# Optimization experiments

Measured on AMD Instinct MI355X. Metric: run time of the kernel, lower is better.

## Reference

```python
import jax, jax.numpy as jnp
import numpy as np

N_HEADS = 16
ROPE_BASE = 10000.0


def apply_rope(x):
    # x: [B, H, T, D]; rotate interleaved pairs along last dim, positions along T
    B, H, T, D = x.shape
    half = D // 2
    inv_freq = 1.0 / (ROPE_BASE ** (jnp.arange(0, half, dtype=jnp.float32) * 2.0 / D))
    angles = jnp.arange(T, dtype=jnp.float32)[:, None] * inv_freq[None, :]  # [T, half]
    cos = jnp.cos(angles).astype(x.dtype)  # [T, half]
    sin = jnp.sin(angles).astype(x.dtype)
    xp = x.reshape(B, H, T, half, 2)
    x1, x2 = xp[..., 0], xp[..., 1]
    out = jnp.stack([x1 * cos - x2 * sin, x1 * sin + x2 * cos], axis=-1)
    return out.reshape(B, H, T, D)


def setup_inputs() -> dict:
    key = jax.random.key(0)
    k1, k2, k3 = jax.random.split(key, 3)
    C = 1024
    x = jax.random.normal(k1, (2, 2048, C), dtype=jnp.float32)
    w_qkv = jax.random.normal(k2, (C, 3 * C), dtype=jnp.float32) * (1.0 / np.sqrt(C))
    w_out = jax.random.normal(k3, (C, C), dtype=jnp.float32) * (1.0 / np.sqrt(C))
    return {"x": x, "w_qkv": w_qkv, "w_out": w_out}


def reference(x, w_qkv, w_out):
    B, T, C = x.shape
    H = N_HEADS
    D = C // H
    qkv = (x @ w_qkv).reshape(B, T, 3, H, D)
    q, k, v = qkv[:, :, 0], qkv[:, :, 1], qkv[:, :, 2]  # [B, T, H, D]
    q = jnp.transpose(q, (0, 2, 1, 3))  # [B, H, T, D]
    k = jnp.transpose(k, (0, 2, 1, 3))
    v = jnp.transpose(v, (0, 2, 1, 3))
    q = apply_rope(q)
    k = apply_rope(k)
    scale = 1.0 / np.sqrt(D)
    scores = jnp.einsum('bhqd,bhkd->bhqk', q, k) * scale
    causal = jnp.tril(jnp.ones((T, T), dtype=bool))
    scores = jnp.where(causal, scores, jnp.finfo(scores.dtype).min)
    attn = jax.nn.softmax(scores, axis=-1)
    out = jnp.einsum('bhqk,bhkd->bhqd', attn, v)  # [B, H, T, D]
    out = jnp.transpose(out, (0, 2, 1, 3)).reshape(B, T, C)
    return out @ w_out
```

## Files before the change

kernel.cpp:

```cpp
#include <hip/hip_runtime.h>
#include <hip/hip_bf16.h>

typedef __attribute__((ext_vector_type(8))) short v8s;
typedef __attribute__((ext_vector_type(4))) float v4f;
typedef __attribute__((ext_vector_type(16))) float v16f;

typedef const __attribute__((address_space(1))) void* gas_ptr;
typedef __attribute__((address_space(3))) void* las_ptr;

#define MFMA16(a, b, c) __builtin_amdgcn_mfma_f32_16x16x32_bf16((a), (b), (c), 0, 0, 0)
#define MFMA32(a, b, c) __builtin_amdgcn_mfma_f32_32x32x16_bf16((a), (b), (c), 0, 0, 0)

__device__ __forceinline__ void gload_lds16(const void* g, void* l) {
  __builtin_amdgcn_global_load_lds((gas_ptr)g, (las_ptr)l, 16, 0, 0);
}

__device__ __forceinline__ unsigned short f2bf(float f) {
  unsigned int u = __float_as_uint(f);
  u += 0x7FFFu + ((u >> 16) & 1u);
  return (unsigned short)(u >> 16);
}
__device__ __forceinline__ float bf2f(unsigned short h) {
  return __uint_as_float(((unsigned int)h) << 16);
}

__device__ __forceinline__ unsigned cvt_pk_bf16(float lo, float hi) {
  unsigned r;
  asm("v_cvt_pk_bf16_f32 %0, %1, %2" : "=v"(r) : "v"(lo), "v"(hi));
  return r;
}

__global__ __launch_bounds__(256) void k_convert(const float* __restrict__ in,
                                                 unsigned short* __restrict__ out,
                                                 float2* __restrict__ tab, int n4) {
  if ((int)blockIdx.x >= 4096) {
    int base = ((int)blockIdx.x - 4096) * 256 + threadIdx.x;
#pragma unroll
    for (int e = 0; e < 8; ++e) {
      int n = base * 8 + e;
      int pos = n >> 5, i = n & 31;
      float invf = exp2f(-(float)i * 0.41524101186092034f);
      float ang = (float)pos * invf;
      float s, cc;
      sincosf(ang, &s, &cc);
      tab[n] = make_float2(cc, s);
    }
    return;
  }
  int i = blockIdx.x * 256 + threadIdx.x;
  if (i >= n4) return;
  float4 v = ((const float4*)in)[i];
  ushort4 o;
  o.x = f2bf(v.x); o.y = f2bf(v.y); o.z = f2bf(v.z); o.w = f2bf(v.w);
  ((ushort4*)out)[i] = o;
}

__global__ __launch_bounds__(256) void k_transpose_convert(const float* __restrict__ in,
                                                           unsigned short* __restrict__ out,
                                                           int R, int C) {
  __shared__ __attribute__((aligned(16))) unsigned short tb[64 * 72];
  const int r0 = blockIdx.y * 64, c0 = blockIdx.x * 64;
  const int tid = threadIdx.x;
#pragma unroll
  for (int j = 0; j < 4; ++j) {
    int slot = tid + 256 * j;
    int row = slot >> 4, q4 = (slot & 15) * 4;
    float4 v = *(const float4*)&in[(size_t)(r0 + row) * C + c0 + q4];
    ushort4 o;
    o.x = f2bf(v.x); o.y = f2bf(v.y); o.z = f2bf(v.z); o.w = f2bf(v.w);
    *(ushort4*)&tb[row * 72 + q4] = o;
  }
  __syncthreads();
#pragma unroll
  for (int j = 0; j < 4; ++j) {
    int slot = tid + 256 * j;
    int crow = slot >> 4, t4 = (slot & 15) * 4;
    ushort4 o;
    o.x = tb[(t4 + 0) * 72 + crow];
    o.y = tb[(t4 + 1) * 72 + crow];
    o.z = tb[(t4 + 2) * 72 + crow];
    o.w = tb[(t4 + 3) * 72 + crow];
    *(ushort4*)&out[(size_t)(c0 + crow) * R + r0 + t4] = o;
  }
}

template <bool F32OUT, int BN, int WAVES_M, int WAVES_N>
__global__ __launch_bounds__(256) void k_gemm(const unsigned short* __restrict__ A,
                                              const unsigned short* __restrict__ Bt,
                                              void* __restrict__ Cout,
                                              int M, int N, int K) {
  constexpr int WM = 128 / (WAVES_M * 16);
  constexpr int WN = BN / (WAVES_N * 16);
  __shared__ __attribute__((aligned(16))) unsigned short As[128 * 32];
  __shared__ __attribute__((aligned(16))) unsigned short Bs[BN * 32];
  const int tid = threadIdx.x;
  const int w = tid >> 6, l = tid & 63, g = l >> 4, c = l & 15;
  const int wr = w / WAVES_N, wc = w % WAVES_N;

  const int nwg = gridDim.x * gridDim.y;
  const int orig = blockIdx.y * gridDim.x + blockIdx.x;
  const int wgid = (orig & 7) * (nwg >> 3) + (orig >> 3);
  const int mt = (wgid / gridDim.x) * 128;
  const int nt = (wgid % gridDim.x) * BN;

  const int rowc = l >> 2, kslot = (l & 3) * 8;

  v4f acc[WM][WN];
#pragma unroll
  for (int m = 0; m < WM; ++m)
#pragma unroll
    for (int n = 0; n < WN; ++n) acc[m][n] = (v4f){0.f, 0.f, 0.f, 0.f};

  constexpr int NCHUNK = 8 + BN / 16;
  for (int kt = 0; kt < K; kt += 32) {
    __syncthreads();
#pragma unroll
    for (int ch = 0; ch < NCHUNK; ch += 4) {
      int cc = ch + w;
      if (cc < 8)
        gload_lds16(&A[(size_t)(mt + cc * 16 + rowc) * K + kt + kslot], &As[cc * 512]);
      else
        gload_lds16(&Bt[(size_t)(nt + (cc - 8) * 16 + rowc) * K + kt + kslot],
                    &Bs[(cc - 8) * 512]);
    }
    __syncthreads();
    v8s af[WM], bfr[WN];
#pragma unroll
    for (int m = 0; m < WM; ++m)
      af[m] = *(const v8s*)&As[(wr * (WM * 16) + m * 16 + c) * 32 + g * 8];
#pragma unroll
    for (int n = 0; n < WN; ++n)
      bfr[n] = *(const v8s*)&Bs[(wc * (WN * 16) + n * 16 + c) * 32 + g * 8];
#pragma unroll
    for (int m = 0; m < WM; ++m)
#pragma unroll
      for (int n = 0; n < WN; ++n)
        acc[m][n] = MFMA16(af[m], bfr[n], acc[m][n]);
  }

#pragma unroll
  for (int m = 0; m < WM; ++m)
#pragma unroll
    for (int n = 0; n < WN; ++n)
#pragma unroll
      for (int r = 0; r < 4; ++r) {
        int row = mt + wr * (WM * 16) + m * 16 + g * 4 + r;
        int col = nt + wc * (WN * 16) + n * 16 + c;
        if (F32OUT)
          ((float*)Cout)[(size_t)row * N + col] = acc[m][n][r];
        else
          ((unsigned short*)Cout)[(size_t)row * N + col] = f2bf(acc[m][n][r]);
      }
}

__global__ __launch_bounds__(256) void k_gemm_qkv(const unsigned short* __restrict__ A,
                                                  const unsigned short* __restrict__ Bt,
                                                  const float2* __restrict__ tab,
                                                  unsigned short* __restrict__ qp,
                                                  unsigned short* __restrict__ kp,
                                                  unsigned short* __restrict__ vp) {
  __shared__ __attribute__((aligned(16))) unsigned short As[128 * 32];
  __shared__ __attribute__((aligned(16))) unsigned short Bs[128 * 32];
  __shared__ __attribute__((aligned(16))) unsigned short T[128 * 136];
  const int tid = threadIdx.x;
  const int w = tid >> 6, l = tid & 63, g = l >> 4, c = l & 15;
  const int wr = w >> 1, wc = w & 1;

  const int nwg = 768;
  const int orig = blockIdx.y * 24 + blockIdx.x;
  const int wgid = (orig & 7) * (nwg >> 3) + (orig >> 3);
  const int mt = (wgid / 24) * 128;
  const int nt = (wgid % 24) * 128;

  const int rowc = l >> 2, kslot = (l & 3) * 8;

  v4f acc[4][4];
#pragma unroll
  for (int m = 0; m < 4; ++m)
#pragma unroll
    for (int n = 0; n < 4; ++n) acc[m][n] = (v4f){0.f, 0.f, 0.f, 0.f};

  for (int kt = 0; kt < 1024; kt += 32) {
    __syncthreads();
#pragma unroll
    for (int ch = 0; ch < 16; ch += 4) {
      int cc = ch + w;
      if (cc < 8)
        gload_lds16(&A[(size_t)(mt + cc * 16 + rowc) * 1024 + kt + kslot], &As[cc * 512]);
      else
        gload_lds16(&Bt[(size_t)(nt + (cc - 8) * 16 + rowc) * 1024 + kt + kslot],
                    &Bs[(cc - 8) * 512]);
    }
    __syncthreads();
    v8s af[4], bfr[4];
#pragma unroll
    for (int m = 0; m < 4; ++m)
      af[m] = *(const v8s*)&As[(wr * 64 + m * 16 + c) * 32 + g * 8];
#pragma unroll
    for (int n = 0; n < 4; ++n)
      bfr[n] = *(const v8s*)&Bs[(wc * 64 + n * 16 + c) * 32 + g * 8];
#pragma unroll
    for (int m = 0; m < 4; ++m)
#pragma unroll
      for (int n = 0; n < 4; ++n)
        acc[m][n] = MFMA16(af[m], bfr[n], acc[m][n]);
  }

#pragma unroll
  for (int m = 0; m < 4; ++m)
#pragma unroll
    for (int n = 0; n < 4; ++n)
#pragma unroll
      for (int r = 0; r < 4; ++r)
        T[(wr * 64 + m * 16 + g * 4 + r) * 136 + wc * 64 + n * 16 + c] = f2bf(acc[m][n][r]);
  __syncthreads();

  const int which = nt >> 10;
  const int h0 = (nt & 1023) >> 6;
  const int b = mt >> 11;
  const int posbase = mt & 2047;

  if (which < 2) {
    const float qsc = which ? 1.0f : 0.18033688011112042f;
    unsigned short* dst = which ? kp : qp;
#pragma unroll
    for (int it = 0; it < 8; ++it) {
      int task = it * 256 + tid;
      int c32t = task & 31;
      int grp = task >> 5;
      int hg = grp & 1, kd = (grp >> 1) & 3, tR = (grp >> 3) & 3, hd2 = grp >> 5;
      int row = tR * 32 + c32t;
      int d0 = kd * 16 + hg * 8;
      int pos = posbase + row;
      v8s vq = *(const v8s*)&T[row * 136 + hd2 * 64 + d0];
      union { unsigned short s[8]; v8s v; } uo;
#pragma unroll
      for (int p = 0; p < 4; ++p) {
        float2 sc = tab[pos * 32 + (d0 >> 1) + p];
        float x1 = bf2f((unsigned short)vq[2 * p]);
        float x2 = bf2f((unsigned short)vq[2 * p + 1]);
        uo.s[2 * p]     = f2bf((x1 * sc.x - x2 * sc.y) * qsc);
        uo.s[2 * p + 1] = f2bf((x1 * sc.y + x2 * sc.x) * qsc);
      }
      int bh = b * 16 + h0 + hd2;
      int tileG = pos >> 5;
      *(v8s*)&dst[(size_t)bh * 131072 + (tileG * 4 + kd) * 512 + (hg * 32 + c32t) * 8] = uo.v;
    }
  } else {
#pragma unroll
    for (int it = 0; it < 8; ++it) {
      int task = it * 256 + tid;
      int lp = task & 63;
      int grp = task >> 6;
      int md = grp & 1, kc = (grp >> 1) & 1, tR = (grp >> 2) & 3, hd2 = grp >> 4;
      int hh2 = lp >> 5, c32d = lp & 31;
      int d = md * 32 + c32d;
      int brow = tR * 32 + kc * 16 + hh2 * 4;
      union { unsigned short s[8]; v8s v; } uo;
#pragma unroll
      for (int jh = 0; jh < 2; ++jh)
#pragma unroll
        for (int e = 0; e < 4; ++e)
          uo.s[jh * 4 + e] = T[(brow + jh * 8 + e) * 136 + hd2 * 64 + d];
      int bh = b * 16 + h0 + hd2;
      int tileG = (posbase >> 5) + tR;
      *(v8s*)&vp[(size_t)bh * 131072 + ((tileG * 2 + kc) * 2 + md) * 512 + lp * 8] = uo.v;
    }
  }
}

__global__ __launch_bounds__(64) void k_attn(const unsigned short* __restrict__ qp,
                                             const unsigned short* __restrict__ kp,
                                             const unsigned short* __restrict__ vp,
                                             unsigned short* __restrict__ ao,
                                             char* __restrict__ part) {
  const int bid = (int)blockIdx.x;
  const int xcd = bid & 7, s2 = bid >> 3;
  const int bh = xcd + 8 * (s2 / 160);
  const int idx = 159 - (s2 % 160);
  int j, s;
  if (idx >= 96)      { j = 48 + ((idx - 96) >> 2); s = (idx - 96) & 3; }
  else if (idx >= 48) { j = 32 + (idx - 48) / 3;    s = (idx - 48) % 3; }
  else if (idx >= 16) { j = 16 + ((idx - 16) >> 1); s = (idx - 16) & 1; }
  else                { j = idx;                    s = 0; }
  const int t0 = s * 16;
  const int t1 = (t0 + 16 < j + 1) ? (t0 + 16) : (j + 1);

  const int l = threadIdx.x;
  const int c32 = l & 31, hh = l >> 5;
  const unsigned short* Qb = qp + (size_t)bh * 131072 + j * 4 * 512;
  const unsigned short* Kb = kp + (size_t)bh * 131072;
  const unsigned short* Vb = vp + (size_t)bh * 131072;

  v8s bq[4];
#pragma unroll
  for (int kd = 0; kd < 4; ++kd) bq[kd] = *(const v8s*)&Qb[kd * 512 + l * 8];

  v16f ot0 = {0,0,0,0,0,0,0,0,0,0,0,0,0,0,0,0};
  v16f ot1 = {0,0,0,0,0,0,0,0,0,0,0,0,0,0,0,0};
  float m2 = -1e30f, lsl = 0.f;

  v8s ak[2][4], av[2][2][2];
#pragma unroll
  for (int kd = 0; kd < 4; ++kd) ak[0][kd] = *(const v8s*)&Kb[((size_t)t0 * 4 + kd) * 512 + l * 8];
#pragma unroll
  for (int kc = 0; kc < 2; ++kc)
#pragma unroll
    for (int md = 0; md < 2; ++md)
      av[0][kc][md] = *(const v8s*)&Vb[(((size_t)t0 * 2 + kc) * 2 + md) * 512 + l * 8];
  if (t0 + 1 < t1) {
#pragma unroll
    for (int kd = 0; kd < 4; ++kd)
      ak[1][kd] = *(const v8s*)&Kb[((size_t)(t0 + 1) * 4 + kd) * 512 + l * 8];
#pragma unroll
    for (int kc = 0; kc < 2; ++kc)
#pragma unroll
      for (int md = 0; md < 2; ++md)
        av[1][kc][md] = *(const v8s*)&Vb[(((size_t)(t0 + 1) * 2 + kc) * 2 + md) * 512 + l * 8];
  }

  int t = t0;
  for (; t + 1 < t1; t += 2) {
    v16f st0 = {0,0,0,0,0,0,0,0,0,0,0,0,0,0,0,0};
    v16f st1 = {0,0,0,0,0,0,0,0,0,0,0,0,0,0,0,0};
    __builtin_amdgcn_s_setprio(1);
#pragma unroll
    for (int kd = 0; kd < 4; ++kd) {
      st0 = MFMA32(ak[0][kd], bq[kd], st0);
      st1 = MFMA32(ak[1][kd], bq[kd], st1);
    }
    __builtin_amdgcn_s_setprio(0);

    if (t + 2 < t1) {
#pragma unroll
      for (int kd = 0; kd < 4; ++kd)
        ak[0][kd] = *(const v8s*)&Kb[((size_t)(t + 2) * 4 + kd) * 512 + l * 8];
    }
    if (t + 3 < t1) {
#pragma unroll
      for (int kd = 0; kd < 4; ++kd)
        ak[1][kd] = *(const v8s*)&Kb[((size_t)(t + 3) * 4 + kd) * 512 + l * 8];
    }

    if (t + 1 == j) {
#pragma unroll
      for (int r = 0; r < 16; ++r) {
        int rloc = (r & 3) + 8 * (r >> 2) + 4 * hh;
        st1[r] = (rloc <= c32) ? st1[r] : -1e30f;
      }
    }

    float a0 = fmaxf(fmaxf(st0[0], st0[1]), fmaxf(st0[2], st0[3]));
    float a1 = fmaxf(fmaxf(st0[4], st0[5]), fmaxf(st0[6], st0[7]));
    float a2 = fmaxf(fmaxf(st0[8], st0[9]), fmaxf(st0[10], st0[11]));
    float a3 = fmaxf(fmaxf(st0[12], st0[13]), fmaxf(st0[14], st0[15]));
    float b0 = fmaxf(fmaxf(st1[0], st1[1]), fmaxf(st1[2], st1[3]));
    float b1 = fmaxf(fmaxf(st1[4], st1[5]), fmaxf(st1[6], st1[7]));
    float b2 = fmaxf(fmaxf(st1[8], st1[9]), fmaxf(st1[10], st1[11]));
    float b3 = fmaxf(fmaxf(st1[12], st1[13]), fmaxf(st1[14], st1[15]));
    float pm = fmaxf(fmaxf(fmaxf(a0, a1), fmaxf(a2, a3)),
                     fmaxf(fmaxf(b0, b1), fmaxf(b2, b3)));
    if (!__all(pm <= m2 + 8.f)) {
      float pmw = fmaxf(pm, __shfl_xor(pm, 32));
      float mn = fmaxf(m2, pmw);
      float al = exp2f(m2 - mn);
      m2 = mn;
      lsl *= al;
      ot0 *= al;
      ot1 *= al;
    }

#pragma unroll
    for (int r = 0; r < 16; ++r) st0[r] = exp2f(st0[r] - m2);
#pragma unroll
    for (int r = 0; r < 16; ++r) st1[r] = exp2f(st1[r] - m2);
    {
      float e0 = (st0[0] + st0[1]) + (st0[2] + st0[3]);
      float e1 = (st0[4] + st0[5]) + (st0[6] + st0[7]);
      float e2 = (st0[8] + st0[9]) + (st0[10] + st0[11]);
      float e3 = (st0[12] + st0[13]) + (st0[14] + st0[15]);
      float f0 = (st1[0] + st1[1]) + (st1[2] + st1[3]);
      float f1 = (st1[4] + st1[5]) + (st1[6] + st1[7]);
      float f2 = (st1[8] + st1[9]) + (st1[10] + st1[11]);
      float f3 = (st1[12] + st1[13]) + (st1[14] + st1[15]);
      lsl += ((e0 + e1) + (e2 + e3)) + ((f0 + f1) + (f2 + f3));
    }

    unsigned wd0[8], wd1[8];
#pragma unroll
    for (int i = 0; i < 8; ++i) wd0[i] = cvt_pk_bf16(st0[2 * i], st0[2 * i + 1]);
#pragma unroll
    for (int i = 0; i < 8; ++i) wd1[i] = cvt_pk_bf16(st1[2 * i], st1[2 * i + 1]);
    union { unsigned u[4]; v8s v; } p00, p01, p10, p11;
    p00.u[0] = wd0[0]; p00.u[1] = wd0[1]; p00.u[2] = wd0[2]; p00.u[3] = wd0[3];
    p01.u[0] = wd0[4]; p01.u[1] = wd0[5]; p01.u[2] = wd0[6]; p01.u[3] = wd0[7];
    p10.u[0] = wd1[0]; p10.u[1] = wd1[1]; p10.u[2] = wd1[2]; p10.u[3] = wd1[3];
    p11.u[0] = wd1[4]; p11.u[1] = wd1[5]; p11.u[2] = wd1[6]; p11.u[3] = wd1[7];

    __builtin_amdgcn_s_setprio(1);
    ot0 = MFMA32(av[0][0][0], p00.v, ot0);
    ot1 = MFMA32(av[0][0][1], p00.v, ot1);
    ot0 = MFMA32(av[0][1][0], p01.v, ot0);
    ot1 = MFMA32(av[0][1][1], p01.v, ot1);
    ot0 = MFMA32(av[1][0][0], p10.v, ot0);
    ot1 = MFMA32(av[1][0][1], p10.v, ot1);
    ot0 = MFMA32(av[1][1][0], p11.v, ot0);
    ot1 = MFMA32(av[1][1][1], p11.v, ot1);
    __builtin_amdgcn_s_setprio(0);

    if (t + 2 < t1) {
#pragma unroll
      for (int kc = 0; kc < 2; ++kc)
#pragma unroll
        for (int md = 0; md < 2; ++md)
          av[0][kc][md] = *(const v8s*)&Vb[(((size_t)(t + 2) * 2 + kc) * 2 + md) * 512 + l * 8];
    }
    if (t + 3 < t1) {
#pragma unroll
      for (int kc = 0; kc < 2; ++kc)
#pragma unroll
        for (int md = 0; md < 2; ++md)
          av[1][kc][md] = *(const v8s*)&Vb[(((size_t)(t + 3) * 2 + kc) * 2 + md) * 512 + l * 8];
    }
  }

  if (t < t1) {
    v16f st = {0,0,0,0,0,0,0,0,0,0,0,0,0,0,0,0};
    __builtin_amdgcn_s_setprio(1);
#pragma unroll
    for (int kd = 0; kd < 4; ++kd) st = MFMA32(ak[0][kd], bq[kd], st);
    __builtin_amdgcn_s_setprio(0);

    if (t == j) {
#pragma unroll
      for (int r = 0; r < 16; ++r) {
        int rloc = (r & 3) + 8 * (r >> 2) + 4 * hh;
        st[r] = (rloc <= c32) ? st[r] : -1e30f;
      }
    }

    float a0 = fmaxf(fmaxf(st[0], st[1]), fmaxf(st[2], st[3]));
    float a1 = fmaxf(fmaxf(st[4], st[5]), fmaxf(st[6], st[7]));
    float a2 = fmaxf(fmaxf(st[8], st[9]), fmaxf(st[10], st[11]));
    float a3 = fmaxf(fmaxf(st[12], st[13]), fmaxf(st[14], st[15]));
    float pm = fmaxf(fmaxf(a0, a1), fmaxf(a2, a3));
    if (!__all(pm <= m2 + 8.f)) {
      float pmw = fmaxf(pm, __shfl_xor(pm, 32));
      float mn = fmaxf(m2, pmw);
      float al = exp2f(m2 - mn);
      m2 = mn;
      lsl *= al;
      ot0 *= al;
      ot1 *= al;
    }
#pragma unroll
    for (int r = 0; r < 16; ++r) st[r] = exp2f(st[r] - m2);
    float e0 = (st[0] + st[1]) + (st[2] + st[3]);
    float e1 = (st[4] + st[5]) + (st[6] + st[7]);
    float e2 = (st[8] + st[9]) + (st[10] + st[11]);
    float e3 = (st[12] + st[13]) + (st[14] + st[15]);
    lsl += (e0 + e1) + (e2 + e3);

    unsigned wd[8];
#pragma unroll
    for (int i = 0; i < 8; ++i) wd[i] = cvt_pk_bf16(st[2 * i], st[2 * i + 1]);
    union { unsigned u[4]; v8s v; } pb0, pb1;
    pb0.u[0] = wd[0]; pb0.u[1] = wd[1]; pb0.u[2] = wd[2]; pb0.u[3] = wd[3];
    pb1.u[0] = wd[4]; pb1.u[1] = wd[5]; pb1.u[2] = wd[6]; pb1.u[3] = wd[7];

    __builtin_amdgcn_s_setprio(1);
    ot0 = MFMA32(av[0][0][0], pb0.v, ot0);
    ot1 = MFMA32(av[0][0][1], pb0.v, ot1);
    ot0 = MFMA32(av[0][1][0], pb1.v, ot0);
    ot1 = MFMA32(av[0][1][1], pb1.v, ot1);
    __builtin_amdgcn_s_setprio(0);
  }

  const float ls = lsl + __shfl_xor(lsl, 32);
  const float inv = 1.f / ls;
  if (j < 16) {
    const int b = bh >> 4, hd = bh & 15;
    const int tq = j * 32 + c32;
    unsigned short* aop = ao + (size_t)(b * 2048 + tq) * 1024 + hd * 64;
#pragma unroll
    for (int md = 0; md < 2; ++md)
#pragma unroll
      for (int q = 0; q < 4; ++q) {
        const v16f& o = md ? ot1 : ot0;
        unsigned w0 = cvt_pk_bf16(o[4 * q + 0] * inv, o[4 * q + 1] * inv);
        unsigned w1 = cvt_pk_bf16(o[4 * q + 2] * inv, o[4 * q + 3] * inv);
        int d = md * 32 + 8 * q + 4 * hh;
        *(uint2*)&aop[d] = make_uint2(w0, w1);
      }
  } else {
    char* slot = part + ((size_t)bh * 160 + idx) * 4352;
#pragma unroll
    for (int md = 0; md < 2; ++md)
#pragma unroll
      for (int i = 0; i < 8; ++i) {
        const v16f& o = md ? ot1 : ot0;
        union { _Float16 h[2]; unsigned u; } pk;
        pk.h[0] = (_Float16)(o[2 * i] * inv);
        pk.h[1] = (_Float16)(o[2 * i + 1] * inv);
        *(unsigned*)(slot + ((md * 8 + i) * 64 + l) * 4) = pk.u;
      }
    if (hh == 0) {
      *(float*)(slot + 4096 + c32 * 4) = m2;
      *(float*)(slot + 4224 + c32 * 4) = ls;
    }
  }
}

__global__ __launch_bounds__(64) void k_comb(const char* __restrict__ part,
                                             unsigned short* __restrict__ ao) {
  const int bh = blockIdx.y;
  const int j = 16 + (int)blockIdx.x;
  const int g = j >> 4;
  const int nch = g + 1;
  const int l = threadIdx.x, c32 = l & 31, hh = l >> 5;
  const int baseg = (g == 1) ? 16 : (g == 2) ? 48 : 96;
  const int ord0 = baseg + (j - 16 * g) * nch;
  const char* base = part + (size_t)bh * 160 * 4352;

  float ms[4], lsv[4], wsc[4];
  float mfin = -1e30f;
#pragma unroll
  for (int s = 0; s < 4; ++s) {
    if (s < nch) {
      const char* sl = base + (size_t)(ord0 + s) * 4352;
      ms[s] = *(const float*)(sl + 4096 + c32 * 4);
      lsv[s] = *(const float*)(sl + 4224 + c32 * 4);
      mfin = fmaxf(mfin, ms[s]);
    }
  }
  float lfin = 0.f;
#pragma unroll
  for (int s = 0; s < 4; ++s) {
    if (s < nch) {
      wsc[s] = lsv[s] * exp2f(ms[s] - mfin);
      lfin += wsc[s];
    }
  }
  const float inv = 1.f / lfin;
#pragma unroll
  for (int s = 0; s < 4; ++s)
    if (s < nch) wsc[s] *= inv;

  const int b = bh >> 4, hd = bh & 15;
  const int t = j * 32 + c32;
  unsigned short* aop = ao + (size_t)(b * 2048 + t) * 1024 + hd * 64;
#pragma unroll
  for (int md = 0; md < 2; ++md)
#pragma unroll
    for (int q4 = 0; q4 < 4; ++q4) {
      const int w0 = md * 8 + 2 * q4;
      float a0 = 0.f, a1 = 0.f, a2 = 0.f, a3 = 0.f;
#pragma unroll
      for (int s = 0; s < 4; ++s) {
        if (s < nch) {
          const char* sl = base + (size_t)(ord0 + s) * 4352;
          unsigned u0 = *(const unsigned*)(sl + ((w0 + 0) * 64 + l) * 4);
          unsigned u1 = *(const unsigned*)(sl + ((w0 + 1) * 64 + l) * 4);
          union { unsigned u; _Float16 h[2]; } p0, p1;
          p0.u = u0; p1.u = u1;
          a0 += (float)p0.h[0] * wsc[s];
          a1 += (float)p0.h[1] * wsc[s];
          a2 += (float)p1.h[0] * wsc[s];
          a3 += (float)p1.h[1] * wsc[s];
        }
      }
      unsigned o0 = cvt_pk_bf16(a0, a1);
      unsigned o1 = cvt_pk_bf16(a2, a3);
      int d = md * 32 + 8 * q4 + 4 * hh;
      *(uint2*)&aop[d] = make_uint2(o0, o1);
    }
}

extern "C" void kernel_launch(void* const* d_in, const int* in_sizes, int n_in,
                              void* d_out, int out_size, void* d_ws, size_t ws_size,
                              hipStream_t stream) {
  const float* x     = (const float*)d_in[0];
  const float* w_qkv = (const float*)d_in[1];
  const float* w_out = (const float*)d_in[2];
  float* out = (float*)d_out;

  char* ws = (char*)d_ws;
  unsigned short* xbf = (unsigned short*)(ws);
  unsigned short* wqT = (unsigned short*)(ws + 8388608);
  unsigned short* woT = (unsigned short*)(ws + 14680064);
  float2* tab = (float2*)(ws + 16777216);
  char* part = (char*)(ws + 16777216);
  unsigned short* qp  = (unsigned short*)(ws + 41943040);
  unsigned short* kp  = (unsigned short*)(ws + 50331648);
  unsigned short* vp  = (unsigned short*)(ws + 58720256);

  k_convert<<<4128, 256, 0, stream>>>(x, xbf, tab, 1048576);
  k_transpose_convert<<<dim3(48, 16), 256, 0, stream>>>(w_qkv, wqT, 1024, 3072);
  k_transpose_convert<<<dim3(16, 16), 256, 0, stream>>>(w_out, woT, 1024, 1024);
  k_gemm_qkv<<<dim3(24, 32), 256, 0, stream>>>(xbf, wqT, tab, qp, kp, vp);
  k_attn<<<5120, 64, 0, stream>>>(qp, kp, vp, xbf , part);
  k_comb<<<dim3(48, 32), 64, 0, stream>>>(part, xbf);
  k_gemm<true, 64, 4, 1><<<dim3(16, 32), 256, 0, stream>>>(xbf, woT, (void*)out, 4096, 1024, 1024);
}
```

Measured before the change: 133.3 us.

## Fuse prep kernels and use K=64 swizzled LDS tiles in GEMMs

Merges the x conversion, RoPE table generation and both weight transpose-conversions into one launch, which removes two kernel launches and their gaps. Both GEMMs now stage K=64 per iteration instead of 32, halving the number of barrier pairs, and store tiles in LDS with an XOR swizzle to avoid bank conflicts on fragment reads. The QKV GEMM reuses a single LDS buffer for the staging tiles and the epilogue transpose, with an added barrier to keep that reuse safe, so LDS use per block does not grow. The cost is a larger LDS footprint in the output GEMM.

```diff
diff --git a/kernel.cpp b/kernel.cpp
--- a/kernel.cpp
+++ b/kernel.cpp
@@ -30,37 +30,10 @@
   return r;
 }
 
-__global__ __launch_bounds__(256) void k_convert(const float* __restrict__ in,
-                                                 unsigned short* __restrict__ out,
-                                                 float2* __restrict__ tab, int n4) {
-  if ((int)blockIdx.x >= 4096) {
-    int base = ((int)blockIdx.x - 4096) * 256 + threadIdx.x;
-#pragma unroll
-    for (int e = 0; e < 8; ++e) {
-      int n = base * 8 + e;
-      int pos = n >> 5, i = n & 31;
-      float invf = exp2f(-(float)i * 0.41524101186092034f);
-      float ang = (float)pos * invf;
-      float s, cc;
-      sincosf(ang, &s, &cc);
-      tab[n] = make_float2(cc, s);
-    }
-    return;
-  }
-  int i = blockIdx.x * 256 + threadIdx.x;
-  if (i >= n4) return;
-  float4 v = ((const float4*)in)[i];
-  ushort4 o;
-  o.x = f2bf(v.x); o.y = f2bf(v.y); o.z = f2bf(v.z); o.w = f2bf(v.w);
-  ((ushort4*)out)[i] = o;
-}
-
-__global__ __launch_bounds__(256) void k_transpose_convert(const float* __restrict__ in,
-                                                           unsigned short* __restrict__ out,
-                                                           int R, int C) {
-  __shared__ __attribute__((aligned(16))) unsigned short tb[64 * 72];
-  const int r0 = blockIdx.y * 64, c0 = blockIdx.x * 64;
-  const int tid = threadIdx.x;
+__device__ __forceinline__ void transpose_body(const float* __restrict__ in,
+                                               unsigned short* __restrict__ out,
+                                               int R, int C, int r0, int c0,
+                                               unsigned short* tb, int tid) {
 #pragma unroll
   for (int j = 0; j < 4; ++j) {
     int slot = tid + 256 * j;
@@ -84,6 +57,43 @@
   }
 }
 
+__global__ __launch_bounds__(256) void k_prep(const float* __restrict__ x,
+                                              const float* __restrict__ w_qkv,
+                                              const float* __restrict__ w_out,
+                                              unsigned short* __restrict__ xbf,
+                                              unsigned short* __restrict__ wqT,
+                                              unsigned short* __restrict__ woT,
+                                              float2* __restrict__ tab) {
+  __shared__ __attribute__((aligned(16))) unsigned short tb[64 * 72];
+  const int bid = (int)blockIdx.x;
+  const int tid = threadIdx.x;
+  if (bid < 4096) {
+    int i = bid * 256 + tid;
+    float4 v = ((const float4*)x)[i];
+    ushort4 o;
+    o.x = f2bf(v.x); o.y = f2bf(v.y); o.z = f2bf(v.z); o.w = f2bf(v.w);
+    ((ushort4*)xbf)[i] = o;
+  } else if (bid < 4128) {
+    int base = (bid - 4096) * 256 + tid;
+#pragma unroll
+    for (int e = 0; e < 8; ++e) {
+      int n = base * 8 + e;
+      int pos = n >> 5, i = n & 31;
+      float invf = exp2f(-(float)i * 0.41524101186092034f);
+      float ang = (float)pos * invf;
+      float s, cc;
+      sincosf(ang, &s, &cc);
+      tab[n] = make_float2(cc, s);
+    }
+  } else if (bid < 4896) {
+    int b2 = bid - 4128;
+    transpose_body(w_qkv, wqT, 1024, 3072, (b2 / 48) * 64, (b2 % 48) * 64, tb, tid);
+  } else {
+    int b2 = bid - 4896;
+    transpose_body(w_out, woT, 1024, 1024, (b2 / 16) * 64, (b2 % 16) * 64, tb, tid);
+  }
+}
+
 template <bool F32OUT, int BN, int WAVES_M, int WAVES_N>
 __global__ __launch_bounds__(256) void k_gemm(const unsigned short* __restrict__ A,
                                               const unsigned short* __restrict__ Bt,
@@ -91,8 +101,8 @@
                                               int M, int N, int K) {
   constexpr int WM = 128 / (WAVES_M * 16);
   constexpr int WN = BN / (WAVES_N * 16);
-  __shared__ __attribute__((aligned(16))) unsigned short As[128 * 32];
-  __shared__ __attribute__((aligned(16))) unsigned short Bs[BN * 32];
+  __shared__ __attribute__((aligned(16))) unsigned short As[128 * 64];
+  __shared__ __attribute__((aligned(16))) unsigned short Bs[BN * 64];
   const int tid = threadIdx.x;
   const int w = tid >> 6, l = tid & 63, g = l >> 4, c = l & 15;
   const int wr = w / WAVES_N, wc = w % WAVES_N;
@@ -103,7 +113,8 @@
   const int mt = (wgid / gridDim.x) * 128;
   const int nt = (wgid % gridDim.x) * BN;
 
-  const int rowc = l >> 2, kslot = (l & 3) * 8;
+  const int srow = l >> 3;
+  const int scol = ((l & 7) ^ srow) * 8;
 
   v4f acc[WM][WN];
 #pragma unroll
@@ -111,31 +122,38 @@
 #pragma unroll
     for (int n = 0; n < WN; ++n) acc[m][n] = (v4f){0.f, 0.f, 0.f, 0.f};
 
-  constexpr int NCHUNK = 8 + BN / 16;
-  for (int kt = 0; kt < K; kt += 32) {
+  constexpr int NCHUNK = 16 + BN / 8;
+  for (int kt = 0; kt < K; kt += 64) {
     __syncthreads();
 #pragma unroll
     for (int ch = 0; ch < NCHUNK; ch += 4) {
       int cc = ch + w;
-      if (cc < 8)
-        gload_lds16(&A[(size_t)(mt + cc * 16 + rowc) * K + kt + kslot], &As[cc * 512]);
+      if (cc < 16)
+        gload_lds16(&A[(size_t)(mt + cc * 8 + srow) * K + kt + scol], &As[cc * 512]);
       else
-        gload_lds16(&Bt[(size_t)(nt + (cc - 8) * 16 + rowc) * K + kt + kslot],
-                    &Bs[(cc - 8) * 512]);
+        gload_lds16(&Bt[(size_t)(nt + (cc - 16) * 8 + srow) * K + kt + scol],
+                    &Bs[(cc - 16) * 512]);
     }
     __syncthreads();
-    v8s af[WM], bfr[WN];
-#pragma unroll
-    for (int m = 0; m < WM; ++m)
-      af[m] = *(const v8s*)&As[(wr * (WM * 16) + m * 16 + c) * 32 + g * 8];
-#pragma unroll
-    for (int n = 0; n < WN; ++n)
-      bfr[n] = *(const v8s*)&Bs[(wc * (WN * 16) + n * 16 + c) * 32 + g * 8];
-#pragma unroll
-    for (int m = 0; m < WM; ++m)
-#pragma unroll
-      for (int n = 0; n < WN; ++n)
-        acc[m][n] = MFMA16(af[m], bfr[n], acc[m][n]);
+#pragma unroll
+    for (int kk = 0; kk < 2; ++kk) {
+      v8s af[WM], bfr[WN];
+#pragma unroll
+      for (int m = 0; m < WM; ++m) {
+        int row = wr * (WM * 16) + m * 16 + c;
+        af[m] = *(const v8s*)&As[row * 64 + ((kk * 4 + g) ^ (row & 7)) * 8];
+      }
+#pragma unroll
+      for (int n = 0; n < WN; ++n) {
+        int row = wc * (WN * 16) + n * 16 + c;
+        bfr[n] = *(const v8s*)&Bs[row * 64 + ((kk * 4 + g) ^ (row & 7)) * 8];
+      }
+#pragma unroll
+      for (int m = 0; m < WM; ++m)
+#pragma unroll
+        for (int n = 0; n < WN; ++n)
+          acc[m][n] = MFMA16(af[m], bfr[n], acc[m][n]);
+    }
   }
 
 #pragma unroll
@@ -159,9 +177,7 @@
                                                   unsigned short* __restrict__ qp,
                                                   unsigned short* __restrict__ kp,
                                                   unsigned short* __restrict__ vp) {
-  __shared__ __attribute__((aligned(16))) unsigned short As[128 * 32];
-  __shared__ __attribute__((aligned(16))) unsigned short Bs[128 * 32];
-  __shared__ __attribute__((aligned(16))) unsigned short T[128 * 136];
+  __shared__ __attribute__((aligned(16))) unsigned short lds[128 * 136];
   const int tid = threadIdx.x;
   const int w = tid >> 6, l = tid & 63, g = l >> 4, c = l & 15;
   const int wr = w >> 1, wc = w & 1;
@@ -172,7 +188,8 @@
   const int mt = (wgid / 24) * 128;
   const int nt = (wgid % 24) * 128;
 
-  const int rowc = l >> 2, kslot = (l & 3) * 8;
+  const int srow = l >> 3;
+  const int scol = ((l & 7) ^ srow) * 8;
 
   v4f acc[4][4];
 #pragma unroll
@@ -180,39 +197,47 @@
 #pragma unroll
     for (int n = 0; n < 4; ++n) acc[m][n] = (v4f){0.f, 0.f, 0.f, 0.f};
 
-  for (int kt = 0; kt < 1024; kt += 32) {
+  for (int kt = 0; kt < 1024; kt += 64) {
     __syncthreads();
 #pragma unroll
-    for (int ch = 0; ch < 16; ch += 4) {
+    for (int ch = 0; ch < 32; ch += 4) {
       int cc = ch + w;
-      if (cc < 8)
-        gload_lds16(&A[(size_t)(mt + cc * 16 + rowc) * 1024 + kt + kslot], &As[cc * 512]);
+      if (cc < 16)
+        gload_lds16(&A[(size_t)(mt + cc * 8 + srow) * 1024 + kt + scol], &lds[cc * 512]);
       else
-        gload_lds16(&Bt[(size_t)(nt + (cc - 8) * 16 + rowc) * 1024 + kt + kslot],
-                    &Bs[(cc - 8) * 512]);
+        gload_lds16(&Bt[(size_t)(nt + (cc - 16) * 8 + srow) * 1024 + kt + scol],
+                    &lds[8192 + (cc - 16) * 512]);
     }
     __syncthreads();
-    v8s af[4], bfr[4];
-#pragma unroll
-    for (int m = 0; m < 4; ++m)
-      af[m] = *(const v8s*)&As[(wr * 64 + m * 16 + c) * 32 + g * 8];
+#pragma unroll
+    for (int kk = 0; kk < 2; ++kk) {
+      v8s af[4], bfr[4];
+#pragma unroll
+      for (int m = 0; m < 4; ++m) {
+        int row = wr * 64 + m * 16 + c;
+        af[m] = *(const v8s*)&lds[row * 64 + ((kk * 4 + g) ^ (row & 7)) * 8];
+      }
+#pragma unroll
+      for (int n = 0; n < 4; ++n) {
+        int row = wc * 64 + n * 16 + c;
+        bfr[n] = *(const v8s*)&lds[8192 + row * 64 + ((kk * 4 + g) ^ (row & 7)) * 8];
+      }
+#pragma unroll
+      for (int m = 0; m < 4; ++m)
+#pragma unroll
+        for (int n = 0; n < 4; ++n)
+          acc[m][n] = MFMA16(af[m], bfr[n], acc[m][n]);
+    }
+  }
+
+  __syncthreads();
+#pragma unroll
+  for (int m = 0; m < 4; ++m)
 #pragma unroll
     for (int n = 0; n < 4; ++n)
-      bfr[n] = *(const v8s*)&Bs[(wc * 64 + n * 16 + c) * 32 + g * 8];
-#pragma unroll
-    for (int m = 0; m < 4; ++m)
-#pragma unroll
-      for (int n = 0; n < 4; ++n)
-        acc[m][n] = MFMA16(af[m], bfr[n], acc[m][n]);
-  }
-
-#pragma unroll
-  for (int m = 0; m < 4; ++m)
-#pragma unroll
-    for (int n = 0; n < 4; ++n)
 #pragma unroll
       for (int r = 0; r < 4; ++r)
-        T[(wr * 64 + m * 16 + g * 4 + r) * 136 + wc * 64 + n * 16 + c] = f2bf(acc[m][n][r]);
+        lds[(wr * 64 + m * 16 + g * 4 + r) * 136 + wc * 64 + n * 16 + c] = f2bf(acc[m][n][r]);
   __syncthreads();
 
   const int which = nt >> 10;
@@ -232,7 +257,7 @@
       int row = tR * 32 + c32t;
       int d0 = kd * 16 + hg * 8;
       int pos = posbase + row;
-      v8s vq = *(const v8s*)&T[row * 136 + hd2 * 64 + d0];
+      v8s vq = *(const v8s*)&lds[row * 136 + hd2 * 64 + d0];
       union { unsigned short s[8]; v8s v; } uo;
 #pragma unroll
       for (int p = 0; p < 4; ++p) {
@@ -261,7 +286,7 @@
       for (int jh = 0; jh < 2; ++jh)
 #pragma unroll
         for (int e = 0; e < 4; ++e)
-          uo.s[jh * 4 + e] = T[(brow + jh * 8 + e) * 136 + hd2 * 64 + d];
+          uo.s[jh * 4 + e] = lds[(brow + jh * 8 + e) * 136 + hd2 * 64 + d];
       int bh = b * 16 + h0 + hd2;
       int tileG = (posbase >> 5) + tR;
       *(v8s*)&vp[(size_t)bh * 131072 + ((tileG * 2 + kc) * 2 + md) * 512 + lp * 8] = uo.v;
@@ -594,9 +619,7 @@
   unsigned short* kp  = (unsigned short*)(ws + 50331648);
   unsigned short* vp  = (unsigned short*)(ws + 58720256);
 
-  k_convert<<<4128, 256, 0, stream>>>(x, xbf, tab, 1048576);
-  k_transpose_convert<<<dim3(48, 16), 256, 0, stream>>>(w_qkv, wqT, 1024, 3072);
-  k_transpose_convert<<<dim3(16, 16), 256, 0, stream>>>(w_out, woT, 1024, 1024);
+  k_prep<<<5152, 256, 0, stream>>>(x, w_qkv, w_out, xbf, wqT, woT, tab);
   k_gemm_qkv<<<dim3(24, 32), 256, 0, stream>>>(xbf, wqT, tab, qp, kp, vp);
   k_attn<<<5120, 64, 0, stream>>>(qp, kp, vp, xbf , part);
   k_comb<<<dim3(48, 32), 64, 0, stream>>>(part, xbf);
```

Result: faster. 127.1 us (-4.7%).
